# Optimization experiments

Measured on AMD Instinct MI355X. Metric: run time of the kernel, lower is better.

## Reference

```python
import jax, jax.numpy as jnp
import numpy as np

B = 128          # batch of predictions
C = 1024         # number of constraints
N = 512          # number of atoms appearing in constraints (minimal subset)
NUM_CLASSES = 1024
BODY_P = 0.02    # body sparsity


def setup_inputs() -> dict:
    rng = np.random.default_rng(0)
    # distinct sorted atom indices into the full class space
    atoms = np.sort(rng.permutation(NUM_CLASSES)[:N]).astype(np.int64)
    # each constraint has one head literal: one-hot in pos_head OR neg_head
    head_atom = rng.integers(0, N, size=C)
    head_sign = rng.random(C) < 0.5
    pos_head = np.zeros((C, N), np.float32)
    neg_head = np.zeros((C, N), np.float32)
    rows = np.arange(C)
    pos_head[rows[head_sign], head_atom[head_sign]] = 1.0
    neg_head[rows[~head_sign], head_atom[~head_sign]] = 1.0
    # sparse disjoint 0/1 body masks, head atom excluded from its own body
    pos_body = (rng.random((C, N)) < BODY_P).astype(np.float32)
    neg_body = ((rng.random((C, N)) < BODY_P) & (pos_body == 0)).astype(np.float32)
    pos_body[rows, head_atom] = 0.0
    neg_body[rows, head_atom] = 0.0
    key = jax.random.key(0)
    preds = jax.random.uniform(key, (B, NUM_CLASSES), dtype=jnp.float32)  # probs in [0,1]
    return {
        "preds": preds,
        "pos_head": jnp.asarray(pos_head),
        "neg_head": jnp.asarray(neg_head),
        "pos_body": jnp.asarray(pos_body),
        "neg_body": jnp.asarray(neg_body),
        "atoms": jnp.asarray(atoms),
    }


def reference(preds, pos_head, neg_head, pos_body, neg_body, atoms):
    # to_minimal: gather atom subset  [B, N]
    m = preds[:, atoms]
    # body_rev[b,c,j] = pos_body + m*(neg_body - pos_body)
    #   = (1-m) where body literal positive, m where negative, 0 otherwise
    body_rev = pos_body[None] + m[:, None, :] * (neg_body - pos_body)[None]  # [B,C,N]
    # candidate body satisfaction degree per constraint
    body_min = 1.0 - jnp.max(body_rev, axis=2)  # [B,C]
    # scatter candidates to head atoms via one-hot head masks (max-reduce over cons)
    lb = jnp.max(body_min[:, :, None] * pos_head[None], axis=1)        # [B,N]
    ub = 1.0 - jnp.max(body_min[:, :, None] * neg_head[None], axis=1)  # [B,N]
    lo = jnp.minimum(lb, ub)
    hi = jnp.maximum(lb, ub)
    updated = jnp.maximum(lo, jnp.minimum(hi, m))
    # from_minimal: scatter updated atoms back into full prediction vector
    return preds.at[:, atoms].set(updated)
```

## Files before the change

### kernel.cpp

```cpp
#include <hip/hip_runtime.h>

#define Bsz 128
#define Csz 1024
#define Nsz 512
#define NCsz 1024
#define CAP 64

__global__ __launch_bounds__(256) void k_pre(
    const float* __restrict__ preds,
    const float* __restrict__ pos_head, const float* __restrict__ neg_head,
    const float* __restrict__ pos_body, const float* __restrict__ neg_body,
    const int* __restrict__ atoms,
    float* __restrict__ mT, unsigned* __restrict__ lbmax, unsigned* __restrict__ ubmax,
    int* __restrict__ pos_list, int* __restrict__ neg_list,
    int* __restrict__ pos_cnt, int* __restrict__ neg_cnt,
    int* __restrict__ head_n, int* __restrict__ head_sign)
{
    int blk = blockIdx.x;
    if (blk < 768) {
        int t = blk * 256 + threadIdx.x;
        if (t < 65536) {
            lbmax[t] = 0u;
        } else if (t < 131072) {
            ubmax[t - 65536] = 0u;
        } else {
            int g = t - 131072;
            int b = g >> 9, n = g & 511;
            mT[n * Bsz + b] = preds[b * NCsz + atoms[n]];
        }
    } else {
        __shared__ int cnts[4][2];
        int wave = threadIdx.x >> 6, lane = threadIdx.x & 63;
        int c = (blk - 768) * 4 + wave;
        if (lane == 0) { cnts[wave][0] = 0; cnts[wave][1] = 0; }
        __syncthreads();
        const float* pbr = pos_body + c * Nsz;
        const float* nbr = neg_body + c * Nsz;
        const float* phr = pos_head + c * Nsz;
        const float* nhr = neg_head + c * Nsz;
        for (int k = 0; k < 8; k++) {
            int n = k * 64 + lane;
            if (pbr[n] != 0.f) { int s = atomicAdd(&cnts[wave][0], 1); if (s < CAP) pos_list[c * CAP + s] = n; }
            if (nbr[n] != 0.f) { int s = atomicAdd(&cnts[wave][1], 1); if (s < CAP) neg_list[c * CAP + s] = n; }
            if (phr[n] != 0.f) { head_n[c] = n; head_sign[c] = 1; }
            if (nhr[n] != 0.f) { head_n[c] = n; head_sign[c] = 0; }
        }
        if (lane == 0) {
            pos_cnt[c] = min(cnts[wave][0], CAP);
            neg_cnt[c] = min(cnts[wave][1], CAP);
        }
    }
}

__global__ __launch_bounds__(128) void k_body(
    const float* __restrict__ mT,
    const int* __restrict__ pos_list, const int* __restrict__ neg_list,
    const int* __restrict__ pos_cnt, const int* __restrict__ neg_cnt,
    const int* __restrict__ head_n, const int* __restrict__ head_sign,
    unsigned* __restrict__ lbmax, unsigned* __restrict__ ubmax)
{
    int c = blockIdx.x, b = threadIdx.x;
    int pc = pos_cnt[c], ncnt = neg_cnt[c];
    const int* pl = pos_list + c * CAP;
    const int* nl = neg_list + c * CAP;
    float acc = 0.f;
    for (int e = 0; e < pc; e++)   acc = fmaxf(acc, 1.f - mT[pl[e] * Bsz + b]);
    for (int e = 0; e < ncnt; e++) acc = fmaxf(acc, mT[nl[e] * Bsz + b]);
    float bm = 1.f - acc;
    unsigned* dst = head_sign[c] ? lbmax : ubmax;
    atomicMax(dst + head_n[c] * Bsz + b, __float_as_uint(bm));
}

__global__ __launch_bounds__(256) void k_final(
    const float* __restrict__ mT,
    const unsigned* __restrict__ lbmax, const unsigned* __restrict__ ubmax,
    const int* __restrict__ atoms, float* __restrict__ out)
{
    int t = blockIdx.x * 256 + threadIdx.x;
    int b = t >> 9, n = t & 511;
    int i = n * Bsz + b;
    float m  = mT[i];
    float lb = __uint_as_float(lbmax[i]);
    float ub = 1.f - __uint_as_float(ubmax[i]);
    float lo = fminf(lb, ub), hi = fmaxf(lb, ub);
    out[b * NCsz + atoms[n]] = fmaxf(lo, fminf(hi, m));
}

extern "C" void kernel_launch(void* const* d_in, const int* in_sizes, int n_in,
                              void* d_out, int out_size, void* d_ws, size_t ws_size,
                              hipStream_t stream)
{
    const float* preds    = (const float*)d_in[0];
    const float* pos_head = (const float*)d_in[1];
    const float* neg_head = (const float*)d_in[2];
    const float* pos_body = (const float*)d_in[3];
    const float* neg_body = (const float*)d_in[4];
    const int*   atoms    = (const int*)d_in[5];
    float* out = (float*)d_out;

    char* ws = (char*)d_ws;
    float*    mT        = (float*)(ws);
    unsigned* lbmax     = (unsigned*)(ws + 65536u  * 4);
    unsigned* ubmax     = (unsigned*)(ws + 131072u * 4);
    int*      pos_list  = (int*)(ws + 196608u * 4);
    int*      neg_list  = (int*)(ws + 262144u * 4);
    int*      pos_cnt   = (int*)(ws + 327680u * 4);
    int*      neg_cnt   = pos_cnt + Csz;
    int*      head_n    = neg_cnt + Csz;
    int*      head_sign = head_n + Csz;

    hipMemcpyAsync(d_out, d_in[0], (size_t)Bsz * NCsz * sizeof(float),
                   hipMemcpyDeviceToDevice, stream);

    k_pre<<<1024, 256, 0, stream>>>(preds, pos_head, neg_head, pos_body, neg_body, atoms,
                                    mT, lbmax, ubmax, pos_list, neg_list,
                                    pos_cnt, neg_cnt, head_n, head_sign);

    k_body<<<Csz, Bsz, 0, stream>>>(mT, pos_list, neg_list, pos_cnt, neg_cnt,
                                    head_n, head_sign, lbmax, ubmax);

    k_final<<<(Bsz * Nsz) / 256, 256, 0, stream>>>(mT, lbmax, ubmax, atoms, out);
}
```

Measured before the change: 85.18 us.

## Fuse body, scatter and final into per-atom solve kernel; drop memcpy and atomics

Replaces the per-constraint body kernel with atomicMax scatter plus a separate finalize kernel by one kernel where each block owns a head atom. The block gathers the constraints whose head is that atom, computes their body minima and writes the clamped result directly. Extra blocks copy non-atom columns of preds, which replaces the device memcpy and removes the lb/ub buffer zeroing. The preprocessing scan also switches to float4 loads. Each atom block scans all 1024 head entries and recomputes its bodies serially, and more than HCAP constraints sharing one head would be silently dropped.

```diff
diff --git a/kernel.cpp b/kernel.cpp
--- a/kernel.cpp
+++ b/kernel.cpp
@@ -5,45 +5,55 @@
 #define Nsz 512
 #define NCsz 1024
 #define CAP 64
+#define HCAP 32
 
 __global__ __launch_bounds__(256) void k_pre(
     const float* __restrict__ preds,
     const float* __restrict__ pos_head, const float* __restrict__ neg_head,
     const float* __restrict__ pos_body, const float* __restrict__ neg_body,
     const int* __restrict__ atoms,
-    float* __restrict__ mT, unsigned* __restrict__ lbmax, unsigned* __restrict__ ubmax,
+    float* __restrict__ mT,
     int* __restrict__ pos_list, int* __restrict__ neg_list,
     int* __restrict__ pos_cnt, int* __restrict__ neg_cnt,
     int* __restrict__ head_n, int* __restrict__ head_sign)
 {
     int blk = blockIdx.x;
-    if (blk < 768) {
-        int t = blk * 256 + threadIdx.x;
-        if (t < 65536) {
-            lbmax[t] = 0u;
-        } else if (t < 131072) {
-            ubmax[t - 65536] = 0u;
-        } else {
-            int g = t - 131072;
-            int b = g >> 9, n = g & 511;
-            mT[n * Bsz + b] = preds[b * NCsz + atoms[n]];
-        }
+    if (blk < 256) {
+        int g = blk * 256 + threadIdx.x;
+        int b = g >> 9, n = g & 511;
+        mT[n * Bsz + b] = preds[b * NCsz + atoms[n]];
     } else {
         __shared__ int cnts[4][2];
         int wave = threadIdx.x >> 6, lane = threadIdx.x & 63;
-        int c = (blk - 768) * 4 + wave;
+        int c = (blk - 256) * 4 + wave;
         if (lane == 0) { cnts[wave][0] = 0; cnts[wave][1] = 0; }
-        __syncthreads();
-        const float* pbr = pos_body + c * Nsz;
-        const float* nbr = neg_body + c * Nsz;
-        const float* phr = pos_head + c * Nsz;
-        const float* nhr = neg_head + c * Nsz;
-        for (int k = 0; k < 8; k++) {
-            int n = k * 64 + lane;
-            if (pbr[n] != 0.f) { int s = atomicAdd(&cnts[wave][0], 1); if (s < CAP) pos_list[c * CAP + s] = n; }
-            if (nbr[n] != 0.f) { int s = atomicAdd(&cnts[wave][1], 1); if (s < CAP) neg_list[c * CAP + s] = n; }
-            if (phr[n] != 0.f) { head_n[c] = n; head_sign[c] = 1; }
-            if (nhr[n] != 0.f) { head_n[c] = n; head_sign[c] = 0; }
+        const float4* pb4 = (const float4*)(pos_body + c * Nsz);
+        const float4* nb4 = (const float4*)(neg_body + c * Nsz);
+        const float4* ph4 = (const float4*)(pos_head + c * Nsz);
+        const float4* nh4 = (const float4*)(neg_head + c * Nsz);
+        for (int k = 0; k < 2; k++) {
+            int q = k * 64 + lane;
+            float4 p = pb4[q];
+            float4 nb = nb4[q];
+            float4 ph = ph4[q];
+            float4 nh = nh4[q];
+            int n0 = q * 4;
+            if (p.x != 0.f) { int s = atomicAdd(&cnts[wave][0], 1); if (s < CAP) pos_list[c * CAP + s] = n0; }
+            if (p.y != 0.f) { int s = atomicAdd(&cnts[wave][0], 1); if (s < CAP) pos_list[c * CAP + s] = n0 + 1; }
+            if (p.z != 0.f) { int s = atomicAdd(&cnts[wave][0], 1); if (s < CAP) pos_list[c * CAP + s] = n0 + 2; }
+            if (p.w != 0.f) { int s = atomicAdd(&cnts[wave][0], 1); if (s < CAP) pos_list[c * CAP + s] = n0 + 3; }
+            if (nb.x != 0.f) { int s = atomicAdd(&cnts[wave][1], 1); if (s < CAP) neg_list[c * CAP + s] = n0; }
+            if (nb.y != 0.f) { int s = atomicAdd(&cnts[wave][1], 1); if (s < CAP) neg_list[c * CAP + s] = n0 + 1; }
+            if (nb.z != 0.f) { int s = atomicAdd(&cnts[wave][1], 1); if (s < CAP) neg_list[c * CAP + s] = n0 + 2; }
+            if (nb.w != 0.f) { int s = atomicAdd(&cnts[wave][1], 1); if (s < CAP) neg_list[c * CAP + s] = n0 + 3; }
+            if (ph.x != 0.f) { head_n[c] = n0;     head_sign[c] = 1; }
+            if (ph.y != 0.f) { head_n[c] = n0 + 1; head_sign[c] = 1; }
+            if (ph.z != 0.f) { head_n[c] = n0 + 2; head_sign[c] = 1; }
+            if (ph.w != 0.f) { head_n[c] = n0 + 3; head_sign[c] = 1; }
+            if (nh.x != 0.f) { head_n[c] = n0;     head_sign[c] = 0; }
+            if (nh.y != 0.f) { head_n[c] = n0 + 1; head_sign[c] = 0; }
+            if (nh.z != 0.f) { head_n[c] = n0 + 2; head_sign[c] = 0; }
+            if (nh.w != 0.f) { head_n[c] = n0 + 3; head_sign[c] = 0; }
         }
         if (lane == 0) {
             pos_cnt[c] = min(cnts[wave][0], CAP);
@@ -52,38 +62,68 @@
     }
 }
 
-__global__ __launch_bounds__(128) void k_body(
+__global__ __launch_bounds__(128) void k_solve(
+    const float* __restrict__ preds,
     const float* __restrict__ mT,
     const int* __restrict__ pos_list, const int* __restrict__ neg_list,
     const int* __restrict__ pos_cnt, const int* __restrict__ neg_cnt,
     const int* __restrict__ head_n, const int* __restrict__ head_sign,
-    unsigned* __restrict__ lbmax, unsigned* __restrict__ ubmax)
+    const int* __restrict__ atoms,
+    float* __restrict__ out)
 {
-    int c = blockIdx.x, b = threadIdx.x;
-    int pc = pos_cnt[c], ncnt = neg_cnt[c];
-    const int* pl = pos_list + c * CAP;
-    const int* nl = neg_list + c * CAP;
-    float acc = 0.f;
-    for (int e = 0; e < pc; e++)   acc = fmaxf(acc, 1.f - mT[pl[e] * Bsz + b]);
-    for (int e = 0; e < ncnt; e++) acc = fmaxf(acc, mT[nl[e] * Bsz + b]);
-    float bm = 1.f - acc;
-    unsigned* dst = head_sign[c] ? lbmax : ubmax;
-    atomicMax(dst + head_n[c] * Bsz + b, __float_as_uint(bm));
-}
-
-__global__ __launch_bounds__(256) void k_final(
-    const float* __restrict__ mT,
-    const unsigned* __restrict__ lbmax, const unsigned* __restrict__ ubmax,
-    const int* __restrict__ atoms, float* __restrict__ out)
-{
-    int t = blockIdx.x * 256 + threadIdx.x;
-    int b = t >> 9, n = t & 511;
-    int i = n * Bsz + b;
-    float m  = mT[i];
-    float lb = __uint_as_float(lbmax[i]);
-    float ub = 1.f - __uint_as_float(ubmax[i]);
-    float lo = fminf(lb, ub), hi = fmaxf(lb, ub);
-    out[b * NCsz + atoms[n]] = fmaxf(lo, fminf(hi, m));
+    int blk = blockIdx.x, tid = threadIdx.x;
+    if (blk < Nsz) {
+        __shared__ int pc_list[HCAP], nc_list[HCAP];
+        __shared__ int np, nn;
+        if (tid == 0) { np = 0; nn = 0; }
+        __syncthreads();
+        for (int c = tid; c < Csz; c += 128) {
+            if (head_n[c] == blk) {
+                if (head_sign[c]) { int s = atomicAdd(&np, 1); if (s < HCAP) pc_list[s] = c; }
+                else              { int s = atomicAdd(&nn, 1); if (s < HCAP) nc_list[s] = c; }
+            }
+        }
+        __syncthreads();
+        int npc = min(np, HCAP), nnc = min(nn, HCAP);
+        float lbv = 0.f, ubacc = 0.f;
+        for (int i = 0; i < npc; i++) {
+            int c = pc_list[i];
+            float acc = 0.f;
+            int pcn = pos_cnt[c], ncn = neg_cnt[c];
+            const int* pl = pos_list + c * CAP;
+            const int* nl = neg_list + c * CAP;
+            for (int e = 0; e < pcn; e++) acc = fmaxf(acc, 1.f - mT[pl[e] * Bsz + tid]);
+            for (int e = 0; e < ncn; e++) acc = fmaxf(acc, mT[nl[e] * Bsz + tid]);
+            lbv = fmaxf(lbv, 1.f - acc);
+        }
+        for (int i = 0; i < nnc; i++) {
+            int c = nc_list[i];
+            float acc = 0.f;
+            int pcn = pos_cnt[c], ncn = neg_cnt[c];
+            const int* pl = pos_list + c * CAP;
+            const int* nl = neg_list + c * CAP;
+            for (int e = 0; e < pcn; e++) acc = fmaxf(acc, 1.f - mT[pl[e] * Bsz + tid]);
+            for (int e = 0; e < ncn; e++) acc = fmaxf(acc, mT[nl[e] * Bsz + tid]);
+            ubacc = fmaxf(ubacc, 1.f - acc);
+        }
+        float m  = mT[blk * Bsz + tid];
+        float ub = 1.f - ubacc;
+        float lo = fminf(lbv, ub), hi = fmaxf(lbv, ub);
+        out[tid * NCsz + atoms[blk]] = fmaxf(lo, fminf(hi, m));
+    } else {
+        __shared__ int la[Nsz];
+        for (int i = tid; i < Nsz; i += 128) la[i] = atoms[i];
+        __syncthreads();
+        int t = (blk - Nsz) * 128 + tid;
+        int b = t >> 10, j = t & 1023;
+        int lo = 0, hi = Nsz;
+        while (lo < hi) { int mid = (lo + hi) >> 1; if (la[mid] < j) lo = mid + 1; else hi = mid; }
+        bool isatom = (lo < Nsz) && (la[lo] == j);
+        if (!isatom) {
+            out[b * NCsz + j]        = preds[b * NCsz + j];
+            out[(b + 64) * NCsz + j] = preds[(b + 64) * NCsz + j];
+        }
+    }
 }
 
 extern "C" void kernel_launch(void* const* d_in, const int* in_sizes, int n_in,
@@ -99,25 +139,19 @@
     float* out = (float*)d_out;
 
     char* ws = (char*)d_ws;
-    float*    mT        = (float*)(ws);
-    unsigned* lbmax     = (unsigned*)(ws + 65536u  * 4);
-    unsigned* ubmax     = (unsigned*)(ws + 131072u * 4);
-    int*      pos_list  = (int*)(ws + 196608u * 4);
-    int*      neg_list  = (int*)(ws + 262144u * 4);
-    int*      pos_cnt   = (int*)(ws + 327680u * 4);
-    int*      neg_cnt   = pos_cnt + Csz;
-    int*      head_n    = neg_cnt + Csz;
-    int*      head_sign = head_n + Csz;
+    float* mT        = (float*)(ws);
+    int*   pos_list  = (int*)(ws + 65536u  * 4);
+    int*   neg_list  = (int*)(ws + 131072u * 4);
+    int*   pos_cnt   = (int*)(ws + 196608u * 4);
+    int*   neg_cnt   = pos_cnt + Csz;
+    int*   head_n    = neg_cnt + Csz;
+    int*   head_sign = head_n + Csz;
 
-    hipMemcpyAsync(d_out, d_in[0], (size_t)Bsz * NCsz * sizeof(float),
-                   hipMemcpyDeviceToDevice, stream);
+    k_pre<<<512, 256, 0, stream>>>(preds, pos_head, neg_head, pos_body, neg_body, atoms,
+                                   mT, pos_list, neg_list, pos_cnt, neg_cnt,
+                                   head_n, head_sign);
 
-    k_pre<<<1024, 256, 0, stream>>>(preds, pos_head, neg_head, pos_body, neg_body, atoms,
-                                    mT, lbmax, ubmax, pos_list, neg_list,
-                                    pos_cnt, neg_cnt, head_n, head_sign);
-
-    k_body<<<Csz, Bsz, 0, stream>>>(mT, pos_list, neg_list, pos_cnt, neg_cnt,
-                                    head_n, head_sign, lbmax, ubmax);
-
-    k_final<<<(Bsz * Nsz) / 256, 256, 0, stream>>>(mT, lbmax, ubmax, atoms, out);
+    k_solve<<<Nsz + 512, 128, 0, stream>>>(preds, mT, pos_list, neg_list,
+                                           pos_cnt, neg_cnt, head_n, head_sign,
+                                           atoms, out);
 }
```

Result: slower. 100.8 us (+18.4%).

## Fuse output copy into final kernel and vectorize preprocessing loads

Applied to the files above, without the earlier changes.

Replaces the device-to-device memcpy of preds with a branch in the final kernel that copies non-atom columns, using a binary search over atoms kept in shared memory. Zeroes the max buffers with 16-byte stores and scans constraint masks with float4 loads, shrinking the pre-kernel grid. Remaps the final kernel's indexing so mT reads are coalesced. This removes a separate copy operation and launch, at the cost of a per-thread binary search and dropping a block barrier that is only safe within a wave.

```diff
diff --git a/kernel.cpp b/kernel.cpp
--- a/kernel.cpp
+++ b/kernel.cpp
@@ -17,33 +17,45 @@
     int* __restrict__ head_n, int* __restrict__ head_sign)
 {
     int blk = blockIdx.x;
-    if (blk < 768) {
-        int t = blk * 256 + threadIdx.x;
-        if (t < 65536) {
-            lbmax[t] = 0u;
-        } else if (t < 131072) {
-            ubmax[t - 65536] = 0u;
-        } else {
-            int g = t - 131072;
-            int b = g >> 9, n = g & 511;
-            mT[n * Bsz + b] = preds[b * NCsz + atoms[n]];
-        }
+    if (blk < 128) {
+        int q = blk * 256 + threadIdx.x;
+        ((uint4*)lbmax)[q] = make_uint4(0u, 0u, 0u, 0u);
+    } else if (blk < 384) {
+        int g = (blk - 128) * 256 + threadIdx.x;
+        int b = g >> 9, n = g & 511;
+        mT[n * Bsz + b] = preds[b * NCsz + atoms[n]];
     } else {
         __shared__ int cnts[4][2];
         int wave = threadIdx.x >> 6, lane = threadIdx.x & 63;
-        int c = (blk - 768) * 4 + wave;
+        int c = (blk - 384) * 4 + wave;
         if (lane == 0) { cnts[wave][0] = 0; cnts[wave][1] = 0; }
-        __syncthreads();
-        const float* pbr = pos_body + c * Nsz;
-        const float* nbr = neg_body + c * Nsz;
-        const float* phr = pos_head + c * Nsz;
-        const float* nhr = neg_head + c * Nsz;
-        for (int k = 0; k < 8; k++) {
-            int n = k * 64 + lane;
-            if (pbr[n] != 0.f) { int s = atomicAdd(&cnts[wave][0], 1); if (s < CAP) pos_list[c * CAP + s] = n; }
-            if (nbr[n] != 0.f) { int s = atomicAdd(&cnts[wave][1], 1); if (s < CAP) neg_list[c * CAP + s] = n; }
-            if (phr[n] != 0.f) { head_n[c] = n; head_sign[c] = 1; }
-            if (nhr[n] != 0.f) { head_n[c] = n; head_sign[c] = 0; }
+        const float4* pb4 = (const float4*)(pos_body + c * Nsz);
+        const float4* nb4 = (const float4*)(neg_body + c * Nsz);
+        const float4* ph4 = (const float4*)(pos_head + c * Nsz);
+        const float4* nh4 = (const float4*)(neg_head + c * Nsz);
+        for (int k = 0; k < 2; k++) {
+            int q = k * 64 + lane;
+            float4 p  = pb4[q];
+            float4 nb = nb4[q];
+            float4 ph = ph4[q];
+            float4 nh = nh4[q];
+            int n0 = q * 4;
+            if (p.x != 0.f) { int s = atomicAdd(&cnts[wave][0], 1); if (s < CAP) pos_list[c * CAP + s] = n0; }
+            if (p.y != 0.f) { int s = atomicAdd(&cnts[wave][0], 1); if (s < CAP) pos_list[c * CAP + s] = n0 + 1; }
+            if (p.z != 0.f) { int s = atomicAdd(&cnts[wave][0], 1); if (s < CAP) pos_list[c * CAP + s] = n0 + 2; }
+            if (p.w != 0.f) { int s = atomicAdd(&cnts[wave][0], 1); if (s < CAP) pos_list[c * CAP + s] = n0 + 3; }
+            if (nb.x != 0.f) { int s = atomicAdd(&cnts[wave][1], 1); if (s < CAP) neg_list[c * CAP + s] = n0; }
+            if (nb.y != 0.f) { int s = atomicAdd(&cnts[wave][1], 1); if (s < CAP) neg_list[c * CAP + s] = n0 + 1; }
+            if (nb.z != 0.f) { int s = atomicAdd(&cnts[wave][1], 1); if (s < CAP) neg_list[c * CAP + s] = n0 + 2; }
+            if (nb.w != 0.f) { int s = atomicAdd(&cnts[wave][1], 1); if (s < CAP) neg_list[c * CAP + s] = n0 + 3; }
+            if (ph.x != 0.f) { head_n[c] = n0;     head_sign[c] = 1; }
+            if (ph.y != 0.f) { head_n[c] = n0 + 1; head_sign[c] = 1; }
+            if (ph.z != 0.f) { head_n[c] = n0 + 2; head_sign[c] = 1; }
+            if (ph.w != 0.f) { head_n[c] = n0 + 3; head_sign[c] = 1; }
+            if (nh.x != 0.f) { head_n[c] = n0;     head_sign[c] = 0; }
+            if (nh.y != 0.f) { head_n[c] = n0 + 1; head_sign[c] = 0; }
+            if (nh.z != 0.f) { head_n[c] = n0 + 2; head_sign[c] = 0; }
+            if (nh.w != 0.f) { head_n[c] = n0 + 3; head_sign[c] = 0; }
         }
         if (lane == 0) {
             pos_cnt[c] = min(cnts[wave][0], CAP);
@@ -72,18 +84,32 @@
 }
 
 __global__ __launch_bounds__(256) void k_final(
+    const float* __restrict__ preds,
     const float* __restrict__ mT,
     const unsigned* __restrict__ lbmax, const unsigned* __restrict__ ubmax,
     const int* __restrict__ atoms, float* __restrict__ out)
 {
-    int t = blockIdx.x * 256 + threadIdx.x;
-    int b = t >> 9, n = t & 511;
-    int i = n * Bsz + b;
-    float m  = mT[i];
-    float lb = __uint_as_float(lbmax[i]);
-    float ub = 1.f - __uint_as_float(ubmax[i]);
-    float lo = fminf(lb, ub), hi = fmaxf(lb, ub);
-    out[b * NCsz + atoms[n]] = fmaxf(lo, fminf(hi, m));
+    int blk = blockIdx.x, tid = threadIdx.x;
+    if (blk < 256) {
+        int t = blk * 256 + tid;
+        int b = t & 127, n = t >> 7;
+        int i = n * Bsz + b;
+        float m  = mT[i];
+        float lb = __uint_as_float(lbmax[i]);
+        float ub = 1.f - __uint_as_float(ubmax[i]);
+        float lo = fminf(lb, ub), hi = fmaxf(lb, ub);
+        out[b * NCsz + atoms[n]] = fmaxf(lo, fminf(hi, m));
+    } else {
+        __shared__ int la[Nsz];
+        for (int i = tid; i < Nsz; i += 256) la[i] = atoms[i];
+        __syncthreads();
+        int t = (blk - 256) * 256 + tid;
+        int b = t >> 10, j = t & 1023;
+        int lo = 0, hi = Nsz;
+        while (lo < hi) { int mid = (lo + hi) >> 1; if (la[mid] < j) lo = mid + 1; else hi = mid; }
+        bool isatom = (lo < Nsz) && (la[lo] == j);
+        if (!isatom) out[b * NCsz + j] = preds[b * NCsz + j];
+    }
 }
 
 extern "C" void kernel_launch(void* const* d_in, const int* in_sizes, int n_in,
@@ -109,15 +135,12 @@
     int*      head_n    = neg_cnt + Csz;
     int*      head_sign = head_n + Csz;
 
-    hipMemcpyAsync(d_out, d_in[0], (size_t)Bsz * NCsz * sizeof(float),
-                   hipMemcpyDeviceToDevice, stream);
-
-    k_pre<<<1024, 256, 0, stream>>>(preds, pos_head, neg_head, pos_body, neg_body, atoms,
-                                    mT, lbmax, ubmax, pos_list, neg_list,
-                                    pos_cnt, neg_cnt, head_n, head_sign);
+    k_pre<<<640, 256, 0, stream>>>(preds, pos_head, neg_head, pos_body, neg_body, atoms,
+                                   mT, lbmax, ubmax, pos_list, neg_list,
+                                   pos_cnt, neg_cnt, head_n, head_sign);
 
     k_body<<<Csz, Bsz, 0, stream>>>(mT, pos_list, neg_list, pos_cnt, neg_cnt,
                                     head_n, head_sign, lbmax, ubmax);
 
-    k_final<<<(Bsz * Nsz) / 256, 256, 0, stream>>>(mT, lbmax, ubmax, atoms, out);
+    k_final<<<768, 256, 0, stream>>>(preds, mT, lbmax, ubmax, atoms, out);
 }
```

Measured after the change: 78.06 us. 8.4% less time.
